# Performance work log

Hardware: AMD Instinct MI355X
Metric: run time of the kernel (lower is better)

## Reference

```python
import jax, jax.numpy as jnp
import numpy as np

N_HEAD = 8


def _ln(x, g, b, eps=1e-5):
    m = jnp.mean(x, -1, keepdims=True)
    v = jnp.mean((x - m) ** 2, -1, keepdims=True)
    return (x - m) * jax.lax.rsqrt(v + eps) * g + b


def setup_inputs() -> dict:
    key = jax.random.key(0)
    ks = jax.random.split(key, 8)
    B, S, H = 4, 2048, 1024
    PAD = 512  # trailing all-zero (padded) tokens -> masked keys via sign(sum|x|)==0
    s = 0.02
    x = jax.random.normal(ks[0], (B, S, H), jnp.float32)
    x = x.at[:, S - PAD:, :].set(0.0)
    return {
        "x": x,
        "in_w": jax.random.normal(ks[1], (3 * H, H), jnp.float32) * s,
        "in_b": jnp.zeros((3 * H,), jnp.float32),
        "out_w": jax.random.normal(ks[2], (H, H), jnp.float32) * s,
        "out_b": jnp.zeros((H,), jnp.float32),
        "fc1_w": jax.random.normal(ks[3], (H, H), jnp.float32) * s,
        "fc1_b": jnp.zeros((H,), jnp.float32),
        "fc2_w": jax.random.normal(ks[4], (H, H), jnp.float32) * s,
        "fc2_b": jnp.zeros((H,), jnp.float32),
        "g1": jnp.ones((H,), jnp.float32),
        "b1": jnp.zeros((H,), jnp.float32),
        "g2": jnp.ones((H,), jnp.float32),
        "b2": jnp.zeros((H,), jnp.float32),
    }


def reference(x, in_w, in_b, out_w, out_b, fc1_w, fc1_b, fc2_w, fc2_b, g1, b1, g2, b2):
    B, S, H = x.shape
    d = H // N_HEAD
    # key padding mask (real_time=False path): key masked where sign(sum|x|)==0
    pad = jnp.sum(jnp.abs(x), axis=-1) == 0  # [B, S]
    # fused qkv projection (torch MultiheadAttention in_proj)
    qkv = x @ in_w.T + in_b  # [B, S, 3H]
    q, k, v = jnp.split(qkv, 3, axis=-1)
    to_heads = lambda t: t.reshape(B, S, N_HEAD, d).transpose(0, 2, 1, 3)  # [B,h,S,d]
    q, k, v = to_heads(q), to_heads(k), to_heads(v)
    scale = 1.0 / jnp.sqrt(jnp.asarray(d, x.dtype))
    scores = jnp.einsum('bhqd,bhkd->bhqk', q, k) * scale  # [B,h,S,S]
    scores = jnp.where(pad[:, None, None, :], -jnp.inf, scores)
    attn = jax.nn.softmax(scores, axis=-1)
    ctx = jnp.einsum('bhqk,bhkd->bhqd', attn, v)
    ctx = ctx.transpose(0, 2, 1, 3).reshape(B, S, H)
    attn_out = ctx @ out_w.T + out_b
    x1 = _ln(attn_out + x, g1, b1)
    ff = jax.nn.relu(x1 @ fc1_w.T + fc1_b) @ fc2_w.T + fc2_b
    return _ln(ff + x1, g2, b2)
```

## Files before the change

kernel.cpp:

```cpp
#include <hip/hip_runtime.h>
#include <cstdint>
#include <cstddef>

#define B_ 4
#define S_ 2048
#define H_ 1024
#define NH 8
#define HD 128
#define MROWS (B_ * S_)

typedef unsigned short u16;
typedef __bf16 bf16x8 __attribute__((ext_vector_type(8)));
typedef float f32x4 __attribute__((ext_vector_type(4)));
typedef float f32x16 __attribute__((ext_vector_type(16)));
typedef unsigned int u32x4 __attribute__((ext_vector_type(4)));

__device__ __forceinline__ u16 f2b(float f) {
    unsigned u = __builtin_bit_cast(unsigned, f);
    u += 0x7FFFu + ((u >> 16) & 1u);
    return (u16)(u >> 16);
}
__device__ __forceinline__ float b2f(u16 h) {
    unsigned u = ((unsigned)h) << 16;
    return __builtin_bit_cast(float, u);
}

__device__ __forceinline__ void llds16(const void* g, void* l) {
    __builtin_amdgcn_global_load_lds(
        (const __attribute__((address_space(1))) unsigned int*)g,
        (__attribute__((address_space(3))) unsigned int*)l,
        16, 0, 0);
}

__device__ __forceinline__ bf16x8 ld16(const u16* p) {
    return *(const bf16x8*)p;
}

__device__ __forceinline__ f32x4 mfma_bf16(bf16x8 a, bf16x8 b, f32x4 c) {
    return __builtin_amdgcn_mfma_f32_16x16x32_bf16(a, b, c, 0, 0, 0);
}
__device__ __forceinline__ f32x16 mfma32(bf16x8 a, bf16x8 b, f32x16 c) {
    return __builtin_amdgcn_mfma_f32_32x32x16_bf16(a, b, c, 0, 0, 0);
}

__global__ void k_f2b(const float* __restrict__ in, u16* __restrict__ out, int n4) {
    int i = blockIdx.x * 256 + threadIdx.x;
    if (i >= n4) return;
    float4 v = ((const float4*)in)[i];
    ushort4 o;
    o.x = f2b(v.x); o.y = f2b(v.y); o.z = f2b(v.z); o.w = f2b(v.w);
    ((ushort4*)out)[i] = o;
}

__global__ void k_xconv(const float* __restrict__ x, u16* __restrict__ xb,
                        float* __restrict__ maskf) {
    const int row = blockIdx.x, t = threadIdx.x;
    float4 v = ((const float4*)(x + (size_t)row * H_))[t];
    ushort4 o;
    o.x = f2b(v.x); o.y = f2b(v.y); o.z = f2b(v.z); o.w = f2b(v.w);
    ((ushort4*)(xb + (size_t)row * H_))[t] = o;
    float sa = fabsf(v.x) + fabsf(v.y) + fabsf(v.z) + fabsf(v.w);
    for (int off = 32; off; off >>= 1) sa += __shfl_xor(sa, off);
    __shared__ float red[4];
    if ((t & 63) == 0) red[t >> 6] = sa;
    __syncthreads();
    if (t == 0)
        maskf[row] = ((red[0] + red[1] + red[2] + red[3]) == 0.0f) ? -1e30f : 0.0f;
}

__global__ void k_tiles(const float* __restrict__ maskf, int* __restrict__ tlist,
                        int* __restrict__ ntl) {
    __shared__ int flags[4][32];
    const int tid = threadIdx.x;
    if (tid < 128) {
        const int b = tid >> 5, t = tid & 31;
        const float* m = maskf + b * S_ + t * 64;
        int any = 0;
        for (int i = 0; i < 64; ++i) any |= (m[i] == 0.0f);
        flags[b][t] = any;
    }
    __syncthreads();
    if (tid < 4) {
        int n = 0;
        for (int t = 0; t < 32; ++t)
            if (flags[tid][t]) tlist[tid * 32 + n++] = t;
        ntl[tid] = n;
    }
}

template <int MODE>
__global__ __launch_bounds__(256, 2) void k_gemm(
    const u16* __restrict__ A, const u16* __restrict__ Bw,
    const float* __restrict__ bias, int N, int K,
    u16* __restrict__ C, u16* __restrict__ qb, u16* __restrict__ kb,
    u16* __restrict__ vT) {
    __shared__ __align__(16) u16 lds[2 * 128 * 64];
    const int tid = threadIdx.x;
    const int wave = tid >> 6, lane = tid & 63;
    const int bn = blockIdx.x, bm = blockIdx.y;
    const int wr = wave >> 1, wc = wave & 1;
    const int r = lane & 15, g = lane >> 4;

    u16* As = lds;
    u16* Bs = lds + 128 * 64;

    f32x4 acc[4][4];
#pragma unroll
    for (int m = 0; m < 4; ++m)
#pragma unroll
        for (int n = 0; n < 4; ++n) acc[m][n] = (f32x4){0.f, 0.f, 0.f, 0.f};

    const u16* Abase = A + (size_t)bm * 128 * K;
    const u16* Bbase = Bw + (size_t)bn * 128 * K;

    for (int k0 = 0; k0 < K; k0 += 64) {
        __syncthreads();
#pragma unroll
        for (int i = 0; i < 4; ++i) {
            const int chunk = i * 256 + tid;
            const int row = chunk >> 3;
            const int slot = chunk & 7;
            const int gq = slot ^ (row & 7);
            llds16(Abase + (size_t)row * K + k0 + gq * 8,
                   As + (i * 256 + wave * 64) * 8);
            llds16(Bbase + (size_t)row * K + k0 + gq * 8,
                   Bs + (i * 256 + wave * 64) * 8);
        }
        __syncthreads();

        bf16x8 af[2][4], bf[2][4];
#pragma unroll
        for (int ks = 0; ks < 2; ++ks) {
#pragma unroll
            for (int m = 0; m < 4; ++m) {
                const int row = wr * 64 + m * 16 + r;
                const int q = (ks * 4 + g) ^ (r & 7);
                af[ks][m] = ld16(As + row * 64 + q * 8);
            }
#pragma unroll
            for (int n = 0; n < 4; ++n) {
                const int row = wc * 64 + n * 16 + r;
                const int q = (ks * 4 + g) ^ (r & 7);
                bf[ks][n] = ld16(Bs + row * 64 + q * 8);
            }
        }
#pragma unroll
        for (int ks = 0; ks < 2; ++ks)
#pragma unroll
            for (int m = 0; m < 4; ++m)
#pragma unroll
                for (int n = 0; n < 4; ++n)
                    acc[m][n] = mfma_bf16(af[ks][m], bf[ks][n], acc[m][n]);
    }

    if constexpr (MODE == 2) {
        const int part = bn >> 3;
        const int h = bn & 7;
#pragma unroll
        for (int n = 0; n < 4; ++n) {
            const int dd = wc * 64 + n * 16 + r;
            const float bv = bias[bn * 128 + dd];
#pragma unroll
            for (int m = 0; m < 4; ++m) {
                const int rm = bm * 128 + wr * 64 + m * 16 + g * 4;
                const int b = rm >> 11;
                const int s0r = rm & 2047;
#pragma unroll
                for (int i = 0; i < 4; ++i) {
                    float v = acc[m][n][i] + bv;
                    if (part == 0) {
                        qb[(((size_t)b * NH + h) * S_ + (s0r + i)) * HD + dd] =
                            f2b(v * 0.08838834764831845f);
                    } else if (part == 1) {
                        kb[(((size_t)b * NH + h) * S_ + (s0r + i)) * HD + dd] = f2b(v);
                    } else {
                        vT[(((size_t)b * NH + h) * HD + dd) * S_ + (s0r + i)] = f2b(v);
                    }
                }
            }
        }
    } else {
#pragma unroll
        for (int n = 0; n < 4; ++n) {
            const int cn = bn * 128 + wc * 64 + n * 16 + r;
            const float bv = bias[cn];
#pragma unroll
            for (int m = 0; m < 4; ++m) {
                const int rm = bm * 128 + wr * 64 + m * 16 + g * 4;
#pragma unroll
                for (int i = 0; i < 4; ++i) {
                    float v = acc[m][n][i] + bv;
                    if (MODE == 1) v = fmaxf(v, 0.f);
                    C[(size_t)(rm + i) * N + cn] = f2b(v);
                }
            }
        }
    }
}

__global__ __launch_bounds__(256, 2) void k_attn(
    const u16* __restrict__ qb, const u16* __restrict__ kb,
    const u16* __restrict__ vT, const float* __restrict__ maskf,
    const int* __restrict__ tlist, const int* __restrict__ ntl,
    u16* __restrict__ ctxb) {
    __shared__ __align__(16) u16 lds[2][16384];
    const int qt = blockIdx.x, bh = blockIdx.y;
    const int b = bh >> 3, h = bh & 7;
    const int tid = threadIdx.x;
    const int w = tid >> 6, lane = tid & 63;
    const int c = lane & 31, hi = lane >> 5;
    const int q0 = qt * 128 + w * 32;

    const u16* Qp = qb + ((size_t)bh * S_ + q0) * HD;
    const u16* Kp = kb + (size_t)bh * S_ * HD;
    const u16* Vp = vT + (size_t)bh * HD * S_;
    const float* mrow = maskf + b * S_;
    const int* tl = tlist + b * 32;
    const int nt = ntl[b];

    bf16x8 qf[8];
#pragma unroll
    for (int ds = 0; ds < 8; ++ds) qf[ds] = ld16(Qp + c * HD + ds * 16 + hi * 8);

    f32x16 ctx[4];
#pragma unroll
    for (int d4 = 0; d4 < 4; ++d4)
#pragma unroll
        for (int i = 0; i < 16; ++i) ctx[d4][i] = 0.f;
    float mrun = -1e30f, lrun = 0.f;

    auto stage = [&](int buf, int t) {
        const int k0 = t * 64;
        u16* Kt = &lds[buf][0];
        u16* Vt = &lds[buf][8192];
#pragma unroll
        for (int i = 0; i < 4; ++i) {
            const int call = w * 4 + i;
            const int row = call * 4 + (lane >> 4);
            const int sg = (lane & 15) ^ (2 * (row & 7));
            llds16(Kp + (size_t)(k0 + row) * HD + sg * 8, Kt + call * 512);
        }
#pragma unroll
        for (int i = 0; i < 4; ++i) {
            const int call = w * 4 + i;
            const int row = call * 8 + (lane >> 3);
            const int sg = (lane & 7) ^ (row & 7);
            llds16(Vp + (size_t)row * S_ + k0 + sg * 8, Vt + call * 512);
        }
    };

    int cur = 0;
    stage(0, tl[0]);
    __syncthreads();

    for (int j = 0; j < nt; ++j) {
        if (j + 1 < nt) stage(cur ^ 1, tl[j + 1]);
        const int k0 = tl[j] * 64;
        const u16* Kt = &lds[cur][0];
        const u16* Vt = &lds[cur][8192];

        f32x4 mk[8];
#pragma unroll
        for (int kk = 0; kk < 2; ++kk)
#pragma unroll
            for (int qd = 0; qd < 4; ++qd)
                mk[kk * 4 + qd] =
                    *(const f32x4*)(mrow + k0 + kk * 32 + qd * 8 + hi * 4);

        f32x16 p[2];
#pragma unroll
        for (int kk = 0; kk < 2; ++kk)
#pragma unroll
            for (int i = 0; i < 16; ++i) p[kk][i] = 0.f;
#pragma unroll
        for (int kk = 0; kk < 2; ++kk) {
            const int rk = kk * 32 + c;
            const int sw = 2 * (rk & 7);
#pragma unroll
            for (int ds = 0; ds < 8; ++ds) {
                bf16x8 kf = ld16(Kt + rk * 128 + ((ds * 2 + hi) ^ sw) * 8);
                p[kk] = mfma32(kf, qf[ds], p[kk]);
            }
        }

#pragma unroll
        for (int kk = 0; kk < 2; ++kk)
#pragma unroll
            for (int qd = 0; qd < 4; ++qd)
#pragma unroll
                for (int i = 0; i < 4; ++i) p[kk][qd * 4 + i] += mk[kk * 4 + qd][i];

        float t8[8];
#pragma unroll
        for (int i = 0; i < 8; ++i)
            t8[i] = fmaxf(fmaxf(p[0][i], p[0][i + 8]),
                          fmaxf(p[1][i], p[1][i + 8]));
        float t4a = fmaxf(t8[0], t8[4]), t4b = fmaxf(t8[1], t8[5]);
        float t4c = fmaxf(t8[2], t8[6]), t4d = fmaxf(t8[3], t8[7]);
        float pmax = fmaxf(fmaxf(t4a, t4b), fmaxf(t4c, t4d));
        pmax = fmaxf(pmax, __shfl_xor(pmax, 32));

        if (!__all(pmax - mrun <= 8.0f)) {
            const float mn = fmaxf(mrun, pmax);
            const float al = __expf(mrun - mn);
            lrun *= al;
#pragma unroll
            for (int d4 = 0; d4 < 4; ++d4)
#pragma unroll
                for (int i = 0; i < 16; ++i) ctx[d4][i] *= al;
            mrun = mn;
        }

#pragma unroll
        for (int kk = 0; kk < 2; ++kk)
#pragma unroll
            for (int i = 0; i < 16; ++i) p[kk][i] = __expf(p[kk][i] - mrun);
        float s8[8];
#pragma unroll
        for (int i = 0; i < 8; ++i)
            s8[i] = (p[0][i] + p[0][i + 8]) + (p[1][i] + p[1][i + 8]);
        float ls = ((s8[0] + s8[4]) + (s8[1] + s8[5])) +
                   ((s8[2] + s8[6]) + (s8[3] + s8[7]));
        ls += __shfl_xor(ls, 32);
        lrun += ls;

        unsigned pk[16], xk[16];
#pragma unroll
        for (int kk = 0; kk < 2; ++kk)
#pragma unroll
            for (int pp = 0; pp < 8; ++pp)
                pk[kk * 8 + pp] = (unsigned)f2b(p[kk][2 * pp]) |
                                  ((unsigned)f2b(p[kk][2 * pp + 1]) << 16);
#pragma unroll
        for (int t = 0; t < 16; ++t) xk[t] = __shfl_xor(pk[t], 32);

        bf16x8 pb[4];
#pragma unroll
        for (int ks = 0; ks < 4; ++ks) {
            const int o = (ks >> 1) * 8 + (ks & 1) * 4;
            u32x4 dw;
            dw[0] = hi ? xk[o + 2] : pk[o];
            dw[1] = hi ? xk[o + 3] : pk[o + 1];
            dw[2] = hi ? pk[o + 2] : xk[o];
            dw[3] = hi ? pk[o + 3] : xk[o + 1];
            pb[ks] = __builtin_bit_cast(bf16x8, dw);
        }

#pragma unroll
        for (int d4 = 0; d4 < 4; ++d4) {
            const int rd = d4 * 32 + c;
            const int sw = rd & 7;
#pragma unroll
            for (int ks = 0; ks < 4; ++ks) {
                bf16x8 vf = ld16(Vt + rd * 64 + ((ks * 2 + hi) ^ sw) * 8);
                ctx[d4] = mfma32(vf, pb[ks], ctx[d4]);
            }
        }
        __syncthreads();
        cur ^= 1;
    }

    const float inv = 1.0f / lrun;
    u16* cw = &lds[0][0] + w * 4352;
#pragma unroll
    for (int d4 = 0; d4 < 4; ++d4)
#pragma unroll
        for (int qd = 0; qd < 4; ++qd) {
            unsigned lo = (unsigned)f2b(ctx[d4][qd * 4 + 0] * inv) |
                          ((unsigned)f2b(ctx[d4][qd * 4 + 1] * inv) << 16);
            unsigned hi2 = (unsigned)f2b(ctx[d4][qd * 4 + 2] * inv) |
                           ((unsigned)f2b(ctx[d4][qd * 4 + 3] * inv) << 16);
            unsigned long long pv = ((unsigned long long)hi2 << 32) | lo;
            *(unsigned long long*)(cw + c * 136 + d4 * 32 + qd * 8 + hi * 4) = pv;
        }
    __syncthreads();
    const int row = lane >> 1, part = lane & 1;
    const u16* src = cw + row * 136 + part * 64;
    u16* dst = ctxb + ((size_t)b * S_ + q0 + row) * H_ + h * HD + part * 64;
#pragma unroll
    for (int u = 0; u < 8; ++u)
        *(u32x4*)(dst + u * 8) = *(const u32x4*)(src + u * 8);
}

template <int RES_BF16, int OUT_BF16>
__global__ void k_ln(const u16* __restrict__ a, const void* __restrict__ res,
                     const float* __restrict__ gam, const float* __restrict__ bet,
                     void* __restrict__ out) {
    const int row = blockIdx.x, t = threadIdx.x;
    float v[4];
    ushort4 av = ((const ushort4*)(a + (size_t)row * H_))[t];
    v[0] = b2f(av.x); v[1] = b2f(av.y); v[2] = b2f(av.z); v[3] = b2f(av.w);
    if constexpr (RES_BF16) {
        ushort4 rv = ((const ushort4*)((const u16*)res + (size_t)row * H_))[t];
        v[0] += b2f(rv.x); v[1] += b2f(rv.y); v[2] += b2f(rv.z); v[3] += b2f(rv.w);
    } else {
        float4 rv = ((const float4*)((const float*)res + (size_t)row * H_))[t];
        v[0] += rv.x; v[1] += rv.y; v[2] += rv.z; v[3] += rv.w;
    }
    float s = v[0] + v[1] + v[2] + v[3];
    float q = v[0] * v[0] + v[1] * v[1] + v[2] * v[2] + v[3] * v[3];
    for (int off = 32; off; off >>= 1) {
        s += __shfl_xor(s, off);
        q += __shfl_xor(q, off);
    }
    __shared__ float red[8];
    if ((t & 63) == 0) {
        red[t >> 6] = s;
        red[4 + (t >> 6)] = q;
    }
    __syncthreads();
    s = red[0] + red[1] + red[2] + red[3];
    q = red[4] + red[5] + red[6] + red[7];
    const float mean = s * (1.f / 1024.f);
    const float var = q * (1.f / 1024.f) - mean * mean;
    const float rinv = rsqrtf(var + 1e-5f);
    float4 gv = ((const float4*)gam)[t];
    float4 bv = ((const float4*)bet)[t];
    float o0 = (v[0] - mean) * rinv * gv.x + bv.x;
    float o1 = (v[1] - mean) * rinv * gv.y + bv.y;
    float o2 = (v[2] - mean) * rinv * gv.z + bv.z;
    float o3 = (v[3] - mean) * rinv * gv.w + bv.w;
    if constexpr (OUT_BF16) {
        ushort4 o;
        o.x = f2b(o0); o.y = f2b(o1); o.z = f2b(o2); o.w = f2b(o3);
        ((ushort4*)((u16*)out + (size_t)row * H_))[t] = o;
    } else {
        float4 o;
        o.x = o0; o.y = o1; o.z = o2; o.w = o3;
        ((float4*)((float*)out + (size_t)row * H_))[t] = o;
    }
}

extern "C" void kernel_launch(void* const* d_in, const int* in_sizes, int n_in,
                              void* d_out, int out_size, void* d_ws, size_t ws_size,
                              hipStream_t stream) {
    const float* x     = (const float*)d_in[0];
    const float* in_w  = (const float*)d_in[1];
    const float* in_b  = (const float*)d_in[2];
    const float* out_w = (const float*)d_in[3];
    const float* out_b = (const float*)d_in[4];
    const float* fc1_w = (const float*)d_in[5];
    const float* fc1_b = (const float*)d_in[6];
    const float* fc2_w = (const float*)d_in[7];
    const float* fc2_b = (const float*)d_in[8];
    const float* g1    = (const float*)d_in[9];
    const float* b1    = (const float*)d_in[10];
    const float* g2    = (const float*)d_in[11];
    const float* b2    = (const float*)d_in[12];

    char* p = (char*)d_ws;
    auto take = [&](size_t bytes) {
        char* q = p;
        p += (bytes + 255) & ~(size_t)255;
        return (void*)q;
    };
    u16* wqkv    = (u16*)take((size_t)3 * H_ * H_ * 2);
    u16* wout    = (u16*)take((size_t)H_ * H_ * 2);
    u16* wfc1    = (u16*)take((size_t)H_ * H_ * 2);
    u16* wfc2    = (u16*)take((size_t)H_ * H_ * 2);
    float* maskf = (float*)take((size_t)MROWS * 4);
    int* tlist   = (int*)take(4 * 32 * sizeof(int));
    int* ntl     = (int*)take(4 * sizeof(int));
    const size_t actb = (size_t)MROWS * H_ * 2;
    u16* regA = (u16*)take(actb);
    u16* regB = (u16*)take(actb);
    u16* regC = (u16*)take(actb);
    u16* regD = (u16*)take(actb);
    u16* regE = (u16*)take(actb);
    u16* regF = (u16*)take(actb);

    k_f2b<<<(3 * H_ * H_ / 4 + 255) / 256, 256, 0, stream>>>(in_w, wqkv, 3 * H_ * H_ / 4);
    k_f2b<<<(H_ * H_ / 4 + 255) / 256, 256, 0, stream>>>(out_w, wout, H_ * H_ / 4);
    k_f2b<<<(H_ * H_ / 4 + 255) / 256, 256, 0, stream>>>(fc1_w, wfc1, H_ * H_ / 4);
    k_f2b<<<(H_ * H_ / 4 + 255) / 256, 256, 0, stream>>>(fc2_w, wfc2, H_ * H_ / 4);
    k_xconv<<<MROWS, 256, 0, stream>>>(x, regA, maskf);
    k_tiles<<<1, 128, 0, stream>>>(maskf, tlist, ntl);

    k_gemm<2><<<dim3(24, 64), 256, 0, stream>>>(regA, wqkv, in_b, 3 * H_, H_,
                                                nullptr, regB, regC, regD);
    k_attn<<<dim3(16, 32), 256, 0, stream>>>(regB, regC, regD, maskf, tlist, ntl,
                                             regE);
    k_gemm<0><<<dim3(8, 64), 256, 0, stream>>>(regE, wout, out_b, H_, H_, regA,
                                               nullptr, nullptr, nullptr);
    k_ln<0, 1><<<MROWS, 256, 0, stream>>>(regA, x, g1, b1, regF);
    k_gemm<1><<<dim3(8, 64), 256, 0, stream>>>(regF, wfc1, fc1_b, H_, H_, regB,
                                               nullptr, nullptr, nullptr);
    k_gemm<0><<<dim3(8, 64), 256, 0, stream>>>(regB, wfc2, fc2_b, H_, H_, regC,
                                               nullptr, nullptr, nullptr);
    k_ln<1, 0><<<MROWS, 256, 0, stream>>>(regC, regF, g2, b2, (float*)d_out);
}
```

Before: 290.6 us.

## Double-buffer GEMM LDS, skip mask adds on full tiles, use exp2 and packed bf16 ops

The GEMM main loop now uses two LDS buffers so the next K-tile is staged while the current one is computed, at the cost of twice the shared memory per block. Attention now folds log2(e) into the Q scale and uses exp2f. It adds the key mask only on tiles flagged as partially masked, uses v_permlane32_swap instead of shuffles to repack P, uses v_cvt_pk_bf16_f32 conversions, sets s_setprio around the MFMA blocks, and changes the K swizzle. The four weight conversions are merged into one launch, and the first LayerNorm now reads the bf16 copy of x rather than fp32 x, which slightly changes the residual precision.

```diff
diff --git a/kernel.cpp b/kernel.cpp
--- a/kernel.cpp
+++ b/kernel.cpp
@@ -24,6 +24,14 @@
     unsigned u = ((unsigned)h) << 16;
     return __builtin_bit_cast(float, u);
 }
+__device__ __forceinline__ unsigned cvtpk(float lo, float hi) {
+    unsigned r;
+    asm("v_cvt_pk_bf16_f32 %0, %1, %2" : "=v"(r) : "v"(lo), "v"(hi));
+    return r;
+}
+__device__ __forceinline__ void perm32(unsigned& a, unsigned& b) {
+    asm("v_permlane32_swap_b32 %0, %1" : "+v"(a), "+v"(b));
+}
 
 __device__ __forceinline__ void llds16(const void* g, void* l) {
     __builtin_amdgcn_global_load_lds(
@@ -43,22 +51,32 @@
     return __builtin_amdgcn_mfma_f32_32x32x16_bf16(a, b, c, 0, 0, 0);
 }
 
-__global__ void k_f2b(const float* __restrict__ in, u16* __restrict__ out, int n4) {
+__global__ void k_f2b_all(const float* __restrict__ w0, const float* __restrict__ w1,
+                          const float* __restrict__ w2, const float* __restrict__ w3,
+                          u16* __restrict__ o0, u16* __restrict__ o1,
+                          u16* __restrict__ o2, u16* __restrict__ o3) {
     int i = blockIdx.x * 256 + threadIdx.x;
-    if (i >= n4) return;
-    float4 v = ((const float4*)in)[i];
-    ushort4 o;
-    o.x = f2b(v.x); o.y = f2b(v.y); o.z = f2b(v.z); o.w = f2b(v.w);
-    ((ushort4*)out)[i] = o;
+    const float* src;
+    u16* dst;
+    if (i < 786432) { src = w0; dst = o0; }
+    else if (i < 1048576) { src = w1; dst = o1; i -= 786432; }
+    else if (i < 1310720) { src = w2; dst = o2; i -= 1048576; }
+    else { src = w3; dst = o3; i -= 1310720; }
+    float4 v = ((const float4*)src)[i];
+    uint2 o;
+    o.x = cvtpk(v.x, v.y);
+    o.y = cvtpk(v.z, v.w);
+    ((uint2*)dst)[i] = o;
 }
 
 __global__ void k_xconv(const float* __restrict__ x, u16* __restrict__ xb,
                         float* __restrict__ maskf) {
     const int row = blockIdx.x, t = threadIdx.x;
     float4 v = ((const float4*)(x + (size_t)row * H_))[t];
-    ushort4 o;
-    o.x = f2b(v.x); o.y = f2b(v.y); o.z = f2b(v.z); o.w = f2b(v.w);
-    ((ushort4*)(xb + (size_t)row * H_))[t] = o;
+    uint2 o;
+    o.x = cvtpk(v.x, v.y);
+    o.y = cvtpk(v.z, v.w);
+    ((uint2*)(xb + (size_t)row * H_))[t] = o;
     float sa = fabsf(v.x) + fabsf(v.y) + fabsf(v.z) + fabsf(v.w);
     for (int off = 32; off; off >>= 1) sa += __shfl_xor(sa, off);
     __shared__ float red[4];
@@ -70,20 +88,22 @@
 
 __global__ void k_tiles(const float* __restrict__ maskf, int* __restrict__ tlist,
                         int* __restrict__ ntl) {
-    __shared__ int flags[4][32];
+    __shared__ int cnt[4][32];
     const int tid = threadIdx.x;
     if (tid < 128) {
         const int b = tid >> 5, t = tid & 31;
         const float* m = maskf + b * S_ + t * 64;
-        int any = 0;
-        for (int i = 0; i < 64; ++i) any |= (m[i] == 0.0f);
-        flags[b][t] = any;
+        int c = 0;
+        for (int i = 0; i < 64; ++i) c += (m[i] == 0.0f);
+        cnt[b][t] = c;
     }
     __syncthreads();
     if (tid < 4) {
         int n = 0;
-        for (int t = 0; t < 32; ++t)
-            if (flags[tid][t]) tlist[tid * 32 + n++] = t;
+        for (int t = 0; t < 32; ++t) {
+            const int c = cnt[tid][t];
+            if (c) tlist[tid * 32 + n++] = t | ((c < 64) ? 0x10000 : 0);
+        }
         ntl[tid] = n;
     }
 }
@@ -94,16 +114,13 @@
     const float* __restrict__ bias, int N, int K,
     u16* __restrict__ C, u16* __restrict__ qb, u16* __restrict__ kb,
     u16* __restrict__ vT) {
-    __shared__ __align__(16) u16 lds[2 * 128 * 64];
+    __shared__ __align__(16) u16 lds[2][2 * 128 * 64];
     const int tid = threadIdx.x;
     const int wave = tid >> 6, lane = tid & 63;
     const int bn = blockIdx.x, bm = blockIdx.y;
     const int wr = wave >> 1, wc = wave & 1;
     const int r = lane & 15, g = lane >> 4;
 
-    u16* As = lds;
-    u16* Bs = lds + 128 * 64;
-
     f32x4 acc[4][4];
 #pragma unroll
     for (int m = 0; m < 4; ++m)
@@ -113,8 +130,9 @@
     const u16* Abase = A + (size_t)bm * 128 * K;
     const u16* Bbase = Bw + (size_t)bn * 128 * K;
 
-    for (int k0 = 0; k0 < K; k0 += 64) {
-        __syncthreads();
+    auto stage = [&](int buf, int k0) {
+        u16* As = &lds[buf][0];
+        u16* Bs = &lds[buf][8192];
 #pragma unroll
         for (int i = 0; i < 4; ++i) {
             const int chunk = i * 256 + tid;
@@ -126,7 +144,15 @@
             llds16(Bbase + (size_t)row * K + k0 + gq * 8,
                    Bs + (i * 256 + wave * 64) * 8);
         }
-        __syncthreads();
+    };
+
+    stage(0, 0);
+    __syncthreads();
+    int cur = 0;
+    for (int k0 = 0; k0 < K; k0 += 64) {
+        if (k0 + 64 < K) stage(cur ^ 1, k0 + 64);
+        const u16* As = &lds[cur][0];
+        const u16* Bs = &lds[cur][8192];
 
         bf16x8 af[2][4], bf[2][4];
 #pragma unroll
@@ -151,11 +177,15 @@
 #pragma unroll
                 for (int n = 0; n < 4; ++n)
                     acc[m][n] = mfma_bf16(af[ks][m], bf[ks][n], acc[m][n]);
+
+        __syncthreads();
+        cur ^= 1;
     }
 
     if constexpr (MODE == 2) {
         const int part = bn >> 3;
         const int h = bn & 7;
+        const float qs = 1.4426950408889634f * 0.08838834764831845f;
 #pragma unroll
         for (int n = 0; n < 4; ++n) {
             const int dd = wc * 64 + n * 16 + r;
@@ -170,7 +200,7 @@
                     float v = acc[m][n][i] + bv;
                     if (part == 0) {
                         qb[(((size_t)b * NH + h) * S_ + (s0r + i)) * HD + dd] =
-                            f2b(v * 0.08838834764831845f);
+                            f2b(v * qs);
                     } else if (part == 1) {
                         kb[(((size_t)b * NH + h) * S_ + (s0r + i)) * HD + dd] = f2b(v);
                     } else {
@@ -237,7 +267,7 @@
         for (int i = 0; i < 4; ++i) {
             const int call = w * 4 + i;
             const int row = call * 4 + (lane >> 4);
-            const int sg = (lane & 15) ^ (2 * (row & 7));
+            const int sg = (lane & 15) ^ (row & 7);
             llds16(Kp + (size_t)(k0 + row) * HD + sg * 8, Kt + call * 512);
         }
 #pragma unroll
@@ -250,45 +280,44 @@
     };
 
     int cur = 0;
-    stage(0, tl[0]);
+    stage(0, tl[0] & 0xFFFF);
     __syncthreads();
 
     for (int j = 0; j < nt; ++j) {
-        if (j + 1 < nt) stage(cur ^ 1, tl[j + 1]);
-        const int k0 = tl[j] * 64;
+        if (j + 1 < nt) stage(cur ^ 1, tl[j + 1] & 0xFFFF);
+        const int ent = tl[j];
+        const int k0 = (ent & 0xFFFF) * 64;
         const u16* Kt = &lds[cur][0];
         const u16* Vt = &lds[cur][8192];
 
-        f32x4 mk[8];
+        f32x16 p[2];
 #pragma unroll
         for (int kk = 0; kk < 2; ++kk)
 #pragma unroll
-            for (int qd = 0; qd < 4; ++qd)
-                mk[kk * 4 + qd] =
-                    *(const f32x4*)(mrow + k0 + kk * 32 + qd * 8 + hi * 4);
-
-        f32x16 p[2];
-#pragma unroll
-        for (int kk = 0; kk < 2; ++kk)
-#pragma unroll
             for (int i = 0; i < 16; ++i) p[kk][i] = 0.f;
+        __builtin_amdgcn_s_setprio(1);
 #pragma unroll
         for (int kk = 0; kk < 2; ++kk) {
             const int rk = kk * 32 + c;
-            const int sw = 2 * (rk & 7);
+            const int sw = rk & 7;
 #pragma unroll
             for (int ds = 0; ds < 8; ++ds) {
                 bf16x8 kf = ld16(Kt + rk * 128 + ((ds * 2 + hi) ^ sw) * 8);
                 p[kk] = mfma32(kf, qf[ds], p[kk]);
             }
         }
-
-#pragma unroll
-        for (int kk = 0; kk < 2; ++kk)
-#pragma unroll
-            for (int qd = 0; qd < 4; ++qd)
-#pragma unroll
-                for (int i = 0; i < 4; ++i) p[kk][qd * 4 + i] += mk[kk * 4 + qd][i];
+        __builtin_amdgcn_s_setprio(0);
+
+        if (ent & 0x10000) {
+#pragma unroll
+            for (int kk = 0; kk < 2; ++kk)
+#pragma unroll
+                for (int qd = 0; qd < 4; ++qd) {
+                    f32x4 mk = *(const f32x4*)(mrow + k0 + kk * 32 + qd * 8 + hi * 4);
+#pragma unroll
+                    for (int i = 0; i < 4; ++i) p[kk][qd * 4 + i] += mk[i];
+                }
+        }
 
         float t8[8];
 #pragma unroll
@@ -302,7 +331,7 @@
 
         if (!__all(pmax - mrun <= 8.0f)) {
             const float mn = fmaxf(mrun, pmax);
-            const float al = __expf(mrun - mn);
+            const float al = exp2f(mrun - mn);
             lrun *= al;
 #pragma unroll
             for (int d4 = 0; d4 < 4; ++d4)
@@ -314,7 +343,7 @@
 #pragma unroll
         for (int kk = 0; kk < 2; ++kk)
 #pragma unroll
-            for (int i = 0; i < 16; ++i) p[kk][i] = __expf(p[kk][i] - mrun);
+            for (int i = 0; i < 16; ++i) p[kk][i] = exp2f(p[kk][i] - mrun);
         float s8[8];
 #pragma unroll
         for (int i = 0; i < 8; ++i)
@@ -324,28 +353,27 @@
         ls += __shfl_xor(ls, 32);
         lrun += ls;
 
-        unsigned pk[16], xk[16];
+        unsigned pk[16];
 #pragma unroll
         for (int kk = 0; kk < 2; ++kk)
 #pragma unroll
             for (int pp = 0; pp < 8; ++pp)
-                pk[kk * 8 + pp] = (unsigned)f2b(p[kk][2 * pp]) |
-                                  ((unsigned)f2b(p[kk][2 * pp + 1]) << 16);
-#pragma unroll
-        for (int t = 0; t < 16; ++t) xk[t] = __shfl_xor(pk[t], 32);
+                pk[kk * 8 + pp] = cvtpk(p[kk][2 * pp], p[kk][2 * pp + 1]);
 
         bf16x8 pb[4];
 #pragma unroll
         for (int ks = 0; ks < 4; ++ks) {
             const int o = (ks >> 1) * 8 + (ks & 1) * 4;
+            unsigned a0 = pk[o + 0], b0 = pk[o + 2];
+            unsigned a1 = pk[o + 1], b1 = pk[o + 3];
+            perm32(a0, b0);
+            perm32(a1, b1);
             u32x4 dw;
-            dw[0] = hi ? xk[o + 2] : pk[o];
-            dw[1] = hi ? xk[o + 3] : pk[o + 1];
-            dw[2] = hi ? pk[o + 2] : xk[o];
-            dw[3] = hi ? pk[o + 3] : xk[o + 1];
+            dw[0] = a0; dw[1] = a1; dw[2] = b0; dw[3] = b1;
             pb[ks] = __builtin_bit_cast(bf16x8, dw);
         }
 
+        __builtin_amdgcn_s_setprio(1);
 #pragma unroll
         for (int d4 = 0; d4 < 4; ++d4) {
             const int rd = d4 * 32 + c;
@@ -356,6 +384,7 @@
                 ctx[d4] = mfma32(vf, pb[ks], ctx[d4]);
             }
         }
+        __builtin_amdgcn_s_setprio(0);
         __syncthreads();
         cur ^= 1;
     }
@@ -366,10 +395,8 @@
     for (int d4 = 0; d4 < 4; ++d4)
 #pragma unroll
         for (int qd = 0; qd < 4; ++qd) {
-            unsigned lo = (unsigned)f2b(ctx[d4][qd * 4 + 0] * inv) |
-                          ((unsigned)f2b(ctx[d4][qd * 4 + 1] * inv) << 16);
-            unsigned hi2 = (unsigned)f2b(ctx[d4][qd * 4 + 2] * inv) |
-                           ((unsigned)f2b(ctx[d4][qd * 4 + 3] * inv) << 16);
+            unsigned lo = cvtpk(ctx[d4][qd * 4 + 0] * inv, ctx[d4][qd * 4 + 1] * inv);
+            unsigned hi2 = cvtpk(ctx[d4][qd * 4 + 2] * inv, ctx[d4][qd * 4 + 3] * inv);
             unsigned long long pv = ((unsigned long long)hi2 << 32) | lo;
             *(unsigned long long*)(cw + c * 136 + d4 * 32 + qd * 8 + hi * 4) = pv;
         }
@@ -382,21 +409,18 @@
         *(u32x4*)(dst + u * 8) = *(const u32x4*)(src + u * 8);
 }
 
-template <int RES_BF16, int OUT_BF16>
-__global__ void k_ln(const u16* __restrict__ a, const void* __restrict__ res,
+template <int OUT_BF16>
+__global__ void k_ln(const u16* __restrict__ a, const u16* __restrict__ res,
                      const float* __restrict__ gam, const float* __restrict__ bet,
                      void* __restrict__ out) {
     const int row = blockIdx.x, t = threadIdx.x;
     float v[4];
     ushort4 av = ((const ushort4*)(a + (size_t)row * H_))[t];
-    v[0] = b2f(av.x); v[1] = b2f(av.y); v[2] = b2f(av.z); v[3] = b2f(av.w);
-    if constexpr (RES_BF16) {
-        ushort4 rv = ((const ushort4*)((const u16*)res + (size_t)row * H_))[t];
-        v[0] += b2f(rv.x); v[1] += b2f(rv.y); v[2] += b2f(rv.z); v[3] += b2f(rv.w);
-    } else {
-        float4 rv = ((const float4*)((const float*)res + (size_t)row * H_))[t];
-        v[0] += rv.x; v[1] += rv.y; v[2] += rv.z; v[3] += rv.w;
-    }
+    ushort4 rv = ((const ushort4*)(res + (size_t)row * H_))[t];
+    v[0] = b2f(av.x) + b2f(rv.x);
+    v[1] = b2f(av.y) + b2f(rv.y);
+    v[2] = b2f(av.z) + b2f(rv.z);
+    v[3] = b2f(av.w) + b2f(rv.w);
     float s = v[0] + v[1] + v[2] + v[3];
     float q = v[0] * v[0] + v[1] * v[1] + v[2] * v[2] + v[3] * v[3];
     for (int off = 32; off; off >>= 1) {
@@ -421,9 +445,10 @@
     float o2 = (v[2] - mean) * rinv * gv.z + bv.z;
     float o3 = (v[3] - mean) * rinv * gv.w + bv.w;
     if constexpr (OUT_BF16) {
-        ushort4 o;
-        o.x = f2b(o0); o.y = f2b(o1); o.z = f2b(o2); o.w = f2b(o3);
-        ((ushort4*)((u16*)out + (size_t)row * H_))[t] = o;
+        uint2 o;
+        o.x = cvtpk(o0, o1);
+        o.y = cvtpk(o2, o3);
+        ((uint2*)((u16*)out + (size_t)row * H_))[t] = o;
     } else {
         float4 o;
         o.x = o0; o.y = o1; o.z = o2; o.w = o3;
@@ -469,10 +494,8 @@
     u16* regE = (u16*)take(actb);
     u16* regF = (u16*)take(actb);
 
-    k_f2b<<<(3 * H_ * H_ / 4 + 255) / 256, 256, 0, stream>>>(in_w, wqkv, 3 * H_ * H_ / 4);
-    k_f2b<<<(H_ * H_ / 4 + 255) / 256, 256, 0, stream>>>(out_w, wout, H_ * H_ / 4);
-    k_f2b<<<(H_ * H_ / 4 + 255) / 256, 256, 0, stream>>>(fc1_w, wfc1, H_ * H_ / 4);
-    k_f2b<<<(H_ * H_ / 4 + 255) / 256, 256, 0, stream>>>(fc2_w, wfc2, H_ * H_ / 4);
+    k_f2b_all<<<6144, 256, 0, stream>>>(in_w, out_w, fc1_w, fc2_w,
+                                        wqkv, wout, wfc1, wfc2);
     k_xconv<<<MROWS, 256, 0, stream>>>(x, regA, maskf);
     k_tiles<<<1, 128, 0, stream>>>(maskf, tlist, ntl);
 
@@ -480,12 +503,12 @@
                                                 nullptr, regB, regC, regD);
     k_attn<<<dim3(16, 32), 256, 0, stream>>>(regB, regC, regD, maskf, tlist, ntl,
                                              regE);
-    k_gemm<0><<<dim3(8, 64), 256, 0, stream>>>(regE, wout, out_b, H_, H_, regA,
+    k_gemm<0><<<dim3(8, 64), 256, 0, stream>>>(regE, wout, out_b, H_, H_, regB,
                                                nullptr, nullptr, nullptr);
-    k_ln<0, 1><<<MROWS, 256, 0, stream>>>(regA, x, g1, b1, regF);
-    k_gemm<1><<<dim3(8, 64), 256, 0, stream>>>(regF, wfc1, fc1_b, H_, H_, regB,
+    k_ln<1><<<MROWS, 256, 0, stream>>>(regB, regA, g1, b1, regF);
+    k_gemm<1><<<dim3(8, 64), 256, 0, stream>>>(regF, wfc1, fc1_b, H_, H_, regC,
                                                nullptr, nullptr, nullptr);
-    k_gemm<0><<<dim3(8, 64), 256, 0, stream>>>(regB, wfc2, fc2_b, H_, H_, regC,
+    k_gemm<0><<<dim3(8, 64), 256, 0, stream>>>(regC, wfc2, fc2_b, H_, H_, regD,
                                                nullptr, nullptr, nullptr);
-    k_ln<1, 0><<<MROWS, 256, 0, stream>>>(regC, regF, g2, b2, (float*)d_out);
-}
+    k_ln<0><<<MROWS, 256, 0, stream>>>(regD, regF, g2, b2, (float*)d_out);
+}
```

Result: faster. 278.8 us (-4.0%).
